# Optimization experiments

Measured on AMD Instinct MI355X. Metric: run time of the kernel, lower is better.

Reference implementation:

```python
import jax, jax.numpy as jnp
import numpy as np

B, C, H, W, K, NH = 4, 128, 64, 64, 7, 8
DH = C // NH          # per-head dim
PAD = (K - 1) // 2    # symmetric padding since K is odd


def setup_inputs() -> dict:
    key = jax.random.key(0)
    ks = jax.random.split(key, 9)
    s = 1.0 / np.sqrt(C)
    f32 = jnp.float32
    return {
        "x": jax.random.normal(ks[0], (B, C, H, W), f32),
        "wq": jax.random.normal(ks[1], (C, C), f32) * s,
        "bq": jax.random.normal(ks[2], (C,), f32) * 0.01,
        "wk": jax.random.normal(ks[3], (C, C), f32) * s,
        "bk": jax.random.normal(ks[4], (C,), f32) * 0.01,
        "wv": jax.random.normal(ks[5], (C, C), f32) * s,
        "bv": jax.random.normal(ks[6], (C,), f32) * 0.01,
        "pos_h": jax.random.normal(ks[7], (NH, K), f32) * 0.02,
        "pos_w": jax.random.normal(ks[8], (NH, K), f32) * 0.02,
    }


def _unfold(p):
    # p: [B,C,H+K-1,W+K-1] -> [B,C,H,W,K,K] (KxK neighborhood per pixel),
    # matching torch .unfold(2,K,1).unfold(3,K,1). Loop is over fixed kernel size only.
    p1 = jnp.stack([p[:, :, i:i + H, :] for i in range(K)], axis=-1)      # [B,C,H,W+K-1,K]
    return jnp.stack([p1[:, :, :, j:j + W, :] for j in range(K)], axis=-1)  # [B,C,H,W,K,K]


def reference(x, wq, bq, wk, bk, wv, bv, pos_h, pos_w):
    cx = x  # cx defaults to x in the original module
    pc = jnp.pad(cx, ((0, 0), (0, 0), (PAD, PAD), (PAD, PAD)))
    # 1x1 convs are pointwise channel mixes
    k = jnp.einsum('oc,bchw->bohw', wk, pc) + bk[None, :, None, None]
    v = jnp.einsum('oc,bchw->bohw', wv, pc) + bv[None, :, None, None]
    q = jnp.einsum('oc,bchw->bohw', wq, x) + bq[None, :, None, None]

    ku = _unfold(k).reshape(B, NH, DH, H, W, K, K)
    vu = _unfold(v).reshape(B, NH, DH, H, W, K, K)
    qh = q.reshape(B, NH, DH, H, W)

    # per-pixel logits over KxK neighborhood
    logits = jnp.einsum('bndhw,bndhwij->bnhwij', qh, ku)  # [B,NH,H,W,K,K]
    logits = logits + pos_h[None, :, None, None, :, None] + pos_w[None, :, None, None, None, :]

    weights = jax.nn.softmax(logits.reshape(B, NH, H, W, K * K), axis=-1)
    out = jnp.einsum('bnhwk,bndhwk->bndhw', weights, vu.reshape(B, NH, DH, H, W, K * K))
    return out.reshape(B, C, H, W)
```

## Files before the change

kernel.cpp:

```cpp
#include <hip/hip_runtime.h>
#include <cmath>

constexpr int Bn = 4, Cn = 128, Hn = 64, Wn = 64, Kn = 7, NHn = 8, DHn = 16, PADn = 3;
constexpr int HWn = Hn * Wn;
constexpr int TS = 16;
constexpr size_t QPLANE = (size_t)Bn * NHn * HWn * DHn;

constexpr int HR = 22;
constexpr int HC = 24;
constexpr int KP = 24;
constexpr int VW = 14;

typedef float f32x4 __attribute__((ext_vector_type(4)));
typedef short short8 __attribute__((ext_vector_type(8)));
typedef unsigned int u32x4 __attribute__((ext_vector_type(4)));
typedef unsigned short u16x4 __attribute__((ext_vector_type(4)));
typedef unsigned short u16x8 __attribute__((ext_vector_type(8)));

__device__ __forceinline__ unsigned short f32_to_bf16_rne(float f) {
  unsigned u = __float_as_uint(f);
  unsigned r = u + 0x7fffu + ((u >> 16) & 1u);
  return (unsigned short)(r >> 16);
}
__device__ __forceinline__ float bf16_to_f32(unsigned short h) {
  return __uint_as_float(((unsigned)h) << 16);
}
__device__ __forceinline__ unsigned pk_bf16(float lo, float hi) {
  return (__float_as_uint(lo) >> 16) | (__float_as_uint(hi) & 0xffff0000u);
}
__device__ __forceinline__ f32x4 max4(f32x4 a, f32x4 b) {
  a[0] = fmaxf(a[0], b[0]); a[1] = fmaxf(a[1], b[1]);
  a[2] = fmaxf(a[2], b[2]); a[3] = fmaxf(a[3], b[3]);
  return a;
}

union UVcast { u32x4 u; short8 s; };

__global__ __launch_bounds__(256)
void prep(const float* __restrict__ x,
          const float* __restrict__ wq, const float* __restrict__ wk,
          const float* __restrict__ wv,
          unsigned short* __restrict__ Whl, unsigned short* __restrict__ xThl)
{
  const int t = threadIdx.x;
  if (blockIdx.z == 4) {
    if (blockIdx.y != 0 || blockIdx.x >= 48) return;
    const int mat = blockIdx.x >> 4;
    const int chunk = blockIdx.x & 15;
    const float* W = (mat == 0) ? wq : (mat == 1) ? wk : wv;
    const int i = (chunk * 256 + t) * 4;
    const f32x4 v = *reinterpret_cast<const f32x4*>(W + i);
    unsigned short h[4], l[4];
#pragma unroll
    for (int j = 0; j < 4; ++j) {
      h[j] = f32_to_bf16_rne(v[j]);
      l[j] = f32_to_bf16_rne(v[j] - bf16_to_f32(h[j]));
    }
    unsigned short* base = Whl + (size_t)mat * 2 * 16384;
    *reinterpret_cast<uint2*>(base + i) =
        make_uint2(h[0] | ((unsigned)h[1] << 16), h[2] | ((unsigned)h[3] << 16));
    *reinterpret_cast<uint2*>(base + 16384 + i) =
        make_uint2(l[0] | ((unsigned)l[1] << 16), l[2] | ((unsigned)l[3] << 16));
    return;
  }

  __shared__ float sm[32][65];
  const int b   = blockIdx.z;
  const int c0g = blockIdx.y * 32;
  const int p0g = blockIdx.x * 64;
  const float* xb = x + (size_t)b * Cn * HWn;

#pragma unroll
  for (int rep = 0; rep < 2; ++rep) {
    const int cl = rep * 16 + (t >> 4);
    const int pl = (t & 15) * 4;
    const f32x4 v = *reinterpret_cast<const f32x4*>(xb + (size_t)(c0g + cl) * HWn + p0g + pl);
    sm[cl][pl + 0] = v[0]; sm[cl][pl + 1] = v[1];
    sm[cl][pl + 2] = v[2]; sm[cl][pl + 3] = v[3];
  }
  __syncthreads();

  const int pl = t >> 2;
  const int c0 = (t & 3) * 8;
  u32x4 hw, lw;
#pragma unroll
  for (int j = 0; j < 4; ++j) {
    const float v0 = sm[c0 + 2 * j][pl];
    const float v1 = sm[c0 + 2 * j + 1][pl];
    const unsigned short h0 = f32_to_bf16_rne(v0);
    const unsigned short h1 = f32_to_bf16_rne(v1);
    const unsigned short l0 = f32_to_bf16_rne(v0 - bf16_to_f32(h0));
    const unsigned short l1 = f32_to_bf16_rne(v1 - bf16_to_f32(h1));
    hw[j] = h0 | ((unsigned)h1 << 16);
    lw[j] = l0 | ((unsigned)l1 << 16);
  }
  unsigned short* dst = xThl + (size_t)b * 2 * HWn * Cn + (size_t)(p0g + pl) * Cn + c0g + c0;
  *reinterpret_cast<u32x4*>(dst)            = hw;
  *reinterpret_cast<u32x4*>(dst + HWn * Cn) = lw;
}

__global__ __launch_bounds__(64)
void qkv_mfma(const unsigned short* __restrict__ Whl,
              const unsigned short* __restrict__ xThl,
              const float* __restrict__ bq_, const float* __restrict__ bk_,
              const float* __restrict__ bv_,
              unsigned short* __restrict__ qo, unsigned short* __restrict__ kbf,
              unsigned short* __restrict__ vbf)
{
  const int z   = blockIdx.z;
  const int mat = z >> 2;
  const int b   = z & 3;
  const float* bias = (mat == 0) ? bq_ : (mat == 1) ? bk_ : bv_;

  const int lane = threadIdx.x;
  const int r    = lane & 15;
  const int quad = lane >> 4;
  const int mbase = blockIdx.y * 64;
  const int nbase = blockIdx.x * 64;

  const unsigned short* Wm = Whl  + (size_t)mat * 2 * Cn * Cn;
  const unsigned short* Xb = xThl + (size_t)b   * 2 * HWn * Cn;

  f32x4 acc[4][4] = {};

#pragma unroll
  for (int ks = 0; ks < 4; ++ks) {
    const int kk = ks * 32 + quad * 8;
    short8 Ah[4], Al[4], Bh[4], Bl[4];
#pragma unroll
    for (int mt = 0; mt < 4; ++mt) {
      const unsigned short* p = Wm + (size_t)(mbase + mt * 16 + r) * Cn + kk;
      Ah[mt] = *reinterpret_cast<const short8*>(p);
      Al[mt] = *reinterpret_cast<const short8*>(p + Cn * Cn);
    }
#pragma unroll
    for (int nt = 0; nt < 4; ++nt) {
      const unsigned short* p = Xb + (size_t)(nbase + nt * 16 + r) * Cn + kk;
      Bh[nt] = *reinterpret_cast<const short8*>(p);
      Bl[nt] = *reinterpret_cast<const short8*>(p + HWn * Cn);
    }
#pragma unroll
    for (int mt = 0; mt < 4; ++mt)
#pragma unroll
      for (int nt = 0; nt < 4; ++nt) {
        acc[mt][nt] = __builtin_amdgcn_mfma_f32_16x16x32_bf16(Ah[mt], Bh[nt], acc[mt][nt], 0, 0, 0);
        acc[mt][nt] = __builtin_amdgcn_mfma_f32_16x16x32_bf16(Ah[mt], Bl[nt], acc[mt][nt], 0, 0, 0);
        acc[mt][nt] = __builtin_amdgcn_mfma_f32_16x16x32_bf16(Al[mt], Bh[nt], acc[mt][nt], 0, 0, 0);
      }
  }

#pragma unroll
  for (int mt = 0; mt < 4; ++mt) {
    const int n = blockIdx.y * 4 + mt;
    const f32x4 b4 = *reinterpret_cast<const f32x4*>(bias + mbase + mt * 16 + quad * 4);
#pragma unroll
    for (int nt = 0; nt < 4; ++nt) {
      const int p = nbase + nt * 16 + r;
      const size_t off = ((size_t)((b * NHn + n) * HWn + p)) * DHn + quad * 4;
      f32x4 val = acc[mt][nt] + b4;
      if (mat == 0) {
        u16x4 hi4, lo4;
#pragma unroll
        for (int j = 0; j < 4; ++j) {
          const unsigned short hb = f32_to_bf16_rne(val[j]);
          hi4[j] = hb;
          lo4[j] = f32_to_bf16_rne(val[j] - bf16_to_f32(hb));
        }
        *reinterpret_cast<u16x4*>(qo + off)          = hi4;
        *reinterpret_cast<u16x4*>(qo + QPLANE + off) = lo4;
      } else {
        unsigned short* y = (mat == 1) ? kbf : vbf;
        u16x4 pkv;
        pkv[0] = f32_to_bf16_rne(val[0]); pkv[1] = f32_to_bf16_rne(val[1]);
        pkv[2] = f32_to_bf16_rne(val[2]); pkv[3] = f32_to_bf16_rne(val[3]);
        *reinterpret_cast<u16x4*>(y + off) = pkv;
      }
    }
  }
}

__global__ __launch_bounds__(256)
void sasa_attn(const unsigned short* __restrict__ qhl,
               const unsigned short* __restrict__ kbf,
               const unsigned short* __restrict__ vbf,
               const float* __restrict__ bk_, const float* __restrict__ bv_,
               const float* __restrict__ pos_h, const float* __restrict__ pos_w,
               float* __restrict__ out)
{
  __shared__ __align__(16) unsigned short ksm[HR * HC * KP];
  __shared__ __align__(16) unsigned       vsm[HR * DHn * VW];

  const int z  = blockIdx.z;
  const int b  = z >> 3;
  const int n  = z & 7;
  const int h0 = blockIdx.y * TS;
  const int w0 = blockIdx.x * TS;
  const int tid  = threadIdx.x;
  const int lane = tid & 63;
  const int wv   = tid >> 6;
  const int r    = lane & 15;
  const int quad = lane >> 4;
  const int cbase = n * DHn;

  const unsigned short* kb = kbf + ((size_t)(b * NHn + n) * HWn) * DHn;
  const unsigned short* vb = vbf + ((size_t)(b * NHn + n) * HWn) * DHn;
  const size_t qbase = ((size_t)(b * NHn + n) * HWn) * DHn;
  const unsigned short* qhp = qhl + qbase;
  const unsigned short* qlp = qhl + QPLANE + qbase;

  u16x8 kb0, kb1, vb0, vb1;
#pragma unroll
  for (int j = 0; j < 8; ++j) {
    kb0[j] = f32_to_bf16_rne(bk_[cbase + j]);
    kb1[j] = f32_to_bf16_rne(bk_[cbase + 8 + j]);
    vb0[j] = f32_to_bf16_rne(bv_[cbase + j]);
    vb1[j] = f32_to_bf16_rne(bv_[cbase + 8 + j]);
  }

  for (int c = tid; c < HR * HC * 2; c += 256) {
    const int pix  = c >> 1;
    const int half = c & 1;
    const int hh = pix / HC;
    const int ww = pix - hh * HC;
    const int gh = h0 + hh - PADn;
    const int gw = w0 + ww - PADn;
    const bool inb = (gh >= 0) && (gh < Hn) && (gw >= 0) && (gw < Wn);
    u16x8 kd;
    if (inb) kd = *reinterpret_cast<const u16x8*>(kb + ((size_t)(gh * Wn + gw)) * DHn + half * 8);
    else     kd = half ? kb1 : kb0;
    *reinterpret_cast<u16x8*>(ksm + pix * KP + half * 8) = kd;
  }

  for (int pp = tid; pp < HR * (HC / 2); pp += 256) {
    const int hh = pp / (HC / 2);
    const int wp = pp - hh * (HC / 2);
    const int gh = h0 + hh - PADn;
    u16x8 a0, a1, c0, c1;
    {
      const int gw = w0 + 2 * wp - PADn;
      const bool inb = (gh >= 0) && (gh < Hn) && (gw >= 0) && (gw < Wn);
      if (inb) {
        const size_t src = ((size_t)(gh * Wn + gw)) * DHn;
        a0 = *reinterpret_cast<const u16x8*>(vb + src);
        a1 = *reinterpret_cast<const u16x8*>(vb + src + 8);
      } else { a0 = vb0; a1 = vb1; }
    }
    {
      const int gw = w0 + 2 * wp + 1 - PADn;
      const bool inb = (gh >= 0) && (gh < Hn) && (gw >= 0) && (gw < Wn);
      if (inb) {
        const size_t src = ((size_t)(gh * Wn + gw)) * DHn;
        c0 = *reinterpret_cast<const u16x8*>(vb + src);
        c1 = *reinterpret_cast<const u16x8*>(vb + src + 8);
      } else { c0 = vb0; c1 = vb1; }
    }
    unsigned* dst = vsm + (hh * DHn) * VW + wp;
#pragma unroll
    for (int d = 0; d < 8; ++d)
      dst[d * VW] = (unsigned)(unsigned short)a0[d] | ((unsigned)(unsigned short)c0[d] << 16);
#pragma unroll
    for (int d = 0; d < 8; ++d)
      dst[(8 + d) * VW] = (unsigned)(unsigned short)a1[d] | ((unsigned)(unsigned short)c1[d] << 16);
  }

  float ph[7];
#pragma unroll
  for (int i = 0; i < 7; ++i) ph[i] = pos_h[n * Kn + i];
  f32x4 pw4[2];
#pragma unroll
  for (int win = 0; win < 2; ++win) {
#pragma unroll
    for (int reg = 0; reg < 4; ++reg) {
      const int ww = win * 8 + 4 * quad + reg;
      const int j  = ww - r;
      const bool valid = (j >= 0) && (j < 7) && (win == 0 || ww >= 16);
      const int jc = j < 0 ? 0 : (j > 6 ? 6 : j);
      const float pv = pos_w[n * Kn + jc];
      pw4[win][reg] = valid ? pv : -1e30f;
    }
  }

  __syncthreads();

  const f32x4 zero4 = {};
  for (int hl = 0; hl < 4; ++hl) {
    const int h = wv * 4 + hl;

    const int pix = (h0 + h) * Wn + (w0 + r);
    const unsigned short* qsel = (quad < 2) ? qhp : qlp;
    const short8 qf = *reinterpret_cast<const short8*>(qsel + (size_t)pix * DHn + (quad & 1) * 8);

    f32x4 L[14];
#pragma unroll
    for (int i = 0; i < 7; ++i) {
#pragma unroll
      for (int win = 0; win < 2; ++win) {
        const short8 kf = *reinterpret_cast<const short8*>(
            ksm + ((h + i) * HC + win * 8 + r) * KP + (quad & 1) * 8);
        f32x4 d = __builtin_amdgcn_mfma_f32_16x16x32_bf16(kf, qf, zero4, 0, 0, 0);
        d = d + pw4[win];
        d = d + (f32x4)ph[i];
        L[i * 2 + win] = d;
      }
    }

    f32x4 M4 = L[0];
#pragma unroll
    for (int t = 1; t < 14; ++t) M4 = max4(M4, L[t]);
    float m = fmaxf(fmaxf(M4[0], M4[1]), fmaxf(M4[2], M4[3]));
    m = fmaxf(m, __shfl_xor(m, 16, 64));
    m = fmaxf(m, __shfl_xor(m, 32, 64));

    f32x4 S4 = {};
#pragma unroll
    for (int t = 0; t < 14; ++t) {
      f32x4 e;
      e[0] = __expf(L[t][0] - m);
      e[1] = __expf(L[t][1] - m);
      e[2] = __expf(L[t][2] - m);
      e[3] = __expf(L[t][3] - m);
      L[t] = e;
      S4 += e;
    }
    float s = (S4[0] + S4[1]) + (S4[2] + S4[3]);
    s += __shfl_xor(s, 16, 64);
    s += __shfl_xor(s, 32, 64);
    const float inv = 1.0f / s;

    f32x4 oA = {}, oB = {};
#pragma unroll
    for (int i = 0; i < 7; ++i) {
      const f32x4 e0 = L[2 * i]     * (f32x4)inv;
      const f32x4 e1 = L[2 * i + 1] * (f32x4)inv;
      UVcast A;
      A.u[0] = pk_bf16(e0[0], e0[1]);
      A.u[1] = pk_bf16(e0[2], e0[3]);
      A.u[2] = pk_bf16(e1[0], e1[1]);
      A.u[3] = pk_bf16(e1[2], e1[3]);

      const unsigned* vp = vsm + ((h + i) * DHn + r) * VW + 2 * quad;
      const uint2 v0 = *reinterpret_cast<const uint2*>(vp);
      const uint2 v1 = *reinterpret_cast<const uint2*>(vp + 4);
      UVcast Bv;
      Bv.u[0] = v0.x; Bv.u[1] = v0.y; Bv.u[2] = v1.x; Bv.u[3] = v1.y;

      f32x4& acc = (i & 1) ? oB : oA;
      acc = __builtin_amdgcn_mfma_f32_16x16x32_bf16(A.s, Bv.s, acc, 0, 0, 0);
    }
    const f32x4 O = oA + oB;

    float* op = out + ((size_t)(b * Cn + cbase + r)) * HWn + (h0 + h) * Wn + w0 + 4 * quad;
    *reinterpret_cast<f32x4*>(op) = O;
  }
}

extern "C" void kernel_launch(void* const* d_in, const int* in_sizes, int n_in,
                              void* d_out, int out_size, void* d_ws, size_t ws_size,
                              hipStream_t stream) {
  const float* x     = (const float*)d_in[0];
  const float* wq    = (const float*)d_in[1];
  const float* bq    = (const float*)d_in[2];
  const float* wk    = (const float*)d_in[3];
  const float* bk    = (const float*)d_in[4];
  const float* wv    = (const float*)d_in[5];
  const float* bv    = (const float*)d_in[6];
  const float* pos_h = (const float*)d_in[7];
  const float* pos_w = (const float*)d_in[8];
  float* out = (float*)d_out;

  const size_t tensor_elems = (size_t)Bn * Cn * HWn;
  unsigned short* qhl  = (unsigned short*)d_ws;
  unsigned short* kbf  = qhl + 2 * tensor_elems;
  unsigned short* vbf  = kbf + tensor_elems;
  unsigned short* Whl  = vbf + tensor_elems;
  unsigned short* xThl = Whl + (size_t)3 * 2 * Cn * Cn;

  dim3 gp(HWn / 64, Cn / 32, Bn + 1);
  prep<<<gp, 256, 0, stream>>>(x, wq, wk, wv, Whl, xThl);

  dim3 g1(HWn / 64, Cn / 64, 3 * Bn);
  qkv_mfma<<<g1, 64, 0, stream>>>(Whl, xThl, bq, bk, bv, qhl, kbf, vbf);

  dim3 g2(Wn / TS, Hn / TS, Bn * NHn);
  sasa_attn<<<g2, 256, 0, stream>>>(qhl, kbf, vbf, bk, bv, pos_h, pos_w, out);
}
```

Before: 111.5 us.

## Fuse x/weight bf16 split prep into QKV MFMA kernel using LDS-staged x tile

Result: faster. 107.0 us, median of 2 (-4.0%).

```diff
diff --git a/kernel.cpp b/kernel.cpp
--- a/kernel.cpp
+++ b/kernel.cpp
@@ -5,6 +5,9 @@
 constexpr int HWn = Hn * Wn;
 constexpr int TS = 16;
 constexpr size_t QPLANE = (size_t)Bn * NHn * HWn * DHn;
+
+constexpr int SP   = 64;
+constexpr int XROW = 136;
 
 constexpr int HR = 22;
 constexpr int HC = 24;
@@ -36,90 +39,75 @@
 
 union UVcast { u32x4 u; short8 s; };
 
-__global__ __launch_bounds__(256)
-void prep(const float* __restrict__ x,
-          const float* __restrict__ wq, const float* __restrict__ wk,
-          const float* __restrict__ wv,
-          unsigned short* __restrict__ Whl, unsigned short* __restrict__ xThl)
+__global__ __launch_bounds__(512)
+void qkv_fused(const float* __restrict__ x,
+               const float* __restrict__ wq, const float* __restrict__ wk,
+               const float* __restrict__ wv,
+               const float* __restrict__ bq_, const float* __restrict__ bk_,
+               const float* __restrict__ bv_,
+               unsigned short* __restrict__ qo, unsigned short* __restrict__ kbf,
+               unsigned short* __restrict__ vbf)
 {
-  const int t = threadIdx.x;
-  if (blockIdx.z == 4) {
-    if (blockIdx.y != 0 || blockIdx.x >= 48) return;
-    const int mat = blockIdx.x >> 4;
-    const int chunk = blockIdx.x & 15;
-    const float* W = (mat == 0) ? wq : (mat == 1) ? wk : wv;
-    const int i = (chunk * 256 + t) * 4;
-    const f32x4 v = *reinterpret_cast<const f32x4*>(W + i);
-    unsigned short h[4], l[4];
-#pragma unroll
-    for (int j = 0; j < 4; ++j) {
-      h[j] = f32_to_bf16_rne(v[j]);
-      l[j] = f32_to_bf16_rne(v[j] - bf16_to_f32(h[j]));
-    }
-    unsigned short* base = Whl + (size_t)mat * 2 * 16384;
-    *reinterpret_cast<uint2*>(base + i) =
-        make_uint2(h[0] | ((unsigned)h[1] << 16), h[2] | ((unsigned)h[3] << 16));
-    *reinterpret_cast<uint2*>(base + 16384 + i) =
-        make_uint2(l[0] | ((unsigned)l[1] << 16), l[2] | ((unsigned)l[3] << 16));
-    return;
-  }
-
-  __shared__ float sm[32][65];
+  __shared__ float smf[32][SP + 1];
+  __shared__ __align__(16) unsigned short xthi[SP * XROW];
+  __shared__ __align__(16) unsigned short xtlo[SP * XROW];
+
   const int b   = blockIdx.z;
-  const int c0g = blockIdx.y * 32;
-  const int p0g = blockIdx.x * 64;
+  const int p0  = blockIdx.x * SP;
+  const int tid = threadIdx.x;
   const float* xb = x + (size_t)b * Cn * HWn;
 
-#pragma unroll
-  for (int rep = 0; rep < 2; ++rep) {
-    const int cl = rep * 16 + (t >> 4);
-    const int pl = (t & 15) * 4;
-    const f32x4 v = *reinterpret_cast<const f32x4*>(xb + (size_t)(c0g + cl) * HWn + p0g + pl);
-    sm[cl][pl + 0] = v[0]; sm[cl][pl + 1] = v[1];
-    sm[cl][pl + 2] = v[2]; sm[cl][pl + 3] = v[3];
-  }
-  __syncthreads();
-
-  const int pl = t >> 2;
-  const int c0 = (t & 3) * 8;
-  u32x4 hw, lw;
-#pragma unroll
-  for (int j = 0; j < 4; ++j) {
-    const float v0 = sm[c0 + 2 * j][pl];
-    const float v1 = sm[c0 + 2 * j + 1][pl];
-    const unsigned short h0 = f32_to_bf16_rne(v0);
-    const unsigned short h1 = f32_to_bf16_rne(v1);
-    const unsigned short l0 = f32_to_bf16_rne(v0 - bf16_to_f32(h0));
-    const unsigned short l1 = f32_to_bf16_rne(v1 - bf16_to_f32(h1));
-    hw[j] = h0 | ((unsigned)h1 << 16);
-    lw[j] = l0 | ((unsigned)l1 << 16);
-  }
-  unsigned short* dst = xThl + (size_t)b * 2 * HWn * Cn + (size_t)(p0g + pl) * Cn + c0g + c0;
-  *reinterpret_cast<u32x4*>(dst)            = hw;
-  *reinterpret_cast<u32x4*>(dst + HWn * Cn) = lw;
-}
-
-__global__ __launch_bounds__(64)
-void qkv_mfma(const unsigned short* __restrict__ Whl,
-              const unsigned short* __restrict__ xThl,
-              const float* __restrict__ bq_, const float* __restrict__ bk_,
-              const float* __restrict__ bv_,
-              unsigned short* __restrict__ qo, unsigned short* __restrict__ kbf,
-              unsigned short* __restrict__ vbf)
-{
-  const int z   = blockIdx.z;
-  const int mat = z >> 2;
-  const int b   = z & 3;
-  const float* bias = (mat == 0) ? bq_ : (mat == 1) ? bk_ : bv_;
-
-  const int lane = threadIdx.x;
+  f32x4 xr0, xr1, xr2, xr3;
+  {
+    const int c  = tid >> 4;
+    const int p4 = (tid & 15) * 4;
+    const float* bp = xb + (size_t)c * HWn + p0 + p4;
+    xr0 = *reinterpret_cast<const f32x4*>(bp);
+    xr1 = *reinterpret_cast<const f32x4*>(bp + (size_t)32 * HWn);
+    xr2 = *reinterpret_cast<const f32x4*>(bp + (size_t)64 * HWn);
+    xr3 = *reinterpret_cast<const f32x4*>(bp + (size_t)96 * HWn);
+  }
+
+#pragma unroll
+  for (int cc = 0; cc < 4; ++cc) {
+    const f32x4 v = (cc == 0) ? xr0 : (cc == 1) ? xr1 : (cc == 2) ? xr2 : xr3;
+    const int cl = tid >> 4;
+    const int p4 = (tid & 15) * 4;
+    smf[cl][p4 + 0] = v[0]; smf[cl][p4 + 1] = v[1];
+    smf[cl][p4 + 2] = v[2]; smf[cl][p4 + 3] = v[3];
+    __syncthreads();
+    if (tid < 256) {
+      const int pl  = tid >> 2;
+      const int c0l = (tid & 3) * 8;
+      u32x4 hw, lw;
+#pragma unroll
+      for (int j = 0; j < 4; ++j) {
+        const float v0 = smf[c0l + 2 * j][pl];
+        const float v1 = smf[c0l + 2 * j + 1][pl];
+        const unsigned short h0 = f32_to_bf16_rne(v0);
+        const unsigned short h1 = f32_to_bf16_rne(v1);
+        const unsigned short l0 = f32_to_bf16_rne(v0 - bf16_to_f32(h0));
+        const unsigned short l1 = f32_to_bf16_rne(v1 - bf16_to_f32(h1));
+        hw[j] = h0 | ((unsigned)h1 << 16);
+        lw[j] = l0 | ((unsigned)l1 << 16);
+      }
+      const int csw = (cc * 32 + c0l) ^ ((pl & 7) << 3);
+      *reinterpret_cast<u32x4*>(xthi + pl * XROW + csw) = hw;
+      *reinterpret_cast<u32x4*>(xtlo + pl * XROW + csw) = lw;
+    }
+    __syncthreads();
+  }
+
+  const int wave = tid >> 6;
+  if (wave >= 6) return;
+  const int lane = tid & 63;
   const int r    = lane & 15;
   const int quad = lane >> 4;
-  const int mbase = blockIdx.y * 64;
-  const int nbase = blockIdx.x * 64;
-
-  const unsigned short* Wm = Whl  + (size_t)mat * 2 * Cn * Cn;
-  const unsigned short* Xb = xThl + (size_t)b   * 2 * HWn * Cn;
+  const int mat  = wave >> 1;
+  const int half = wave & 1;
+  const int mbase = half * 64;
+  const float* Wsel = (mat == 0) ? wq : (mat == 1) ? wk : wv;
+  const float* bias = (mat == 0) ? bq_ : (mat == 1) ? bk_ : bv_;
 
   f32x4 acc[4][4] = {};
 
@@ -129,15 +117,30 @@
     short8 Ah[4], Al[4], Bh[4], Bl[4];
 #pragma unroll
     for (int mt = 0; mt < 4; ++mt) {
-      const unsigned short* p = Wm + (size_t)(mbase + mt * 16 + r) * Cn + kk;
-      Ah[mt] = *reinterpret_cast<const short8*>(p);
-      Al[mt] = *reinterpret_cast<const short8*>(p + Cn * Cn);
+      const float* wp = Wsel + (size_t)(mbase + mt * 16 + r) * Cn + kk;
+      const f32x4 wa = *reinterpret_cast<const f32x4*>(wp);
+      const f32x4 wb = *reinterpret_cast<const f32x4*>(wp + 4);
+      short8 ah, al;
+#pragma unroll
+      for (int j = 0; j < 4; ++j) {
+        const unsigned short h = f32_to_bf16_rne(wa[j]);
+        ah[j] = (short)h;
+        al[j] = (short)f32_to_bf16_rne(wa[j] - bf16_to_f32(h));
+      }
+#pragma unroll
+      for (int j = 0; j < 4; ++j) {
+        const unsigned short h = f32_to_bf16_rne(wb[j]);
+        ah[4 + j] = (short)h;
+        al[4 + j] = (short)f32_to_bf16_rne(wb[j] - bf16_to_f32(h));
+      }
+      Ah[mt] = ah; Al[mt] = al;
     }
 #pragma unroll
     for (int nt = 0; nt < 4; ++nt) {
-      const unsigned short* p = Xb + (size_t)(nbase + nt * 16 + r) * Cn + kk;
-      Bh[nt] = *reinterpret_cast<const short8*>(p);
-      Bl[nt] = *reinterpret_cast<const short8*>(p + HWn * Cn);
+      const int px  = nt * 16 + r;
+      const int csw = kk ^ ((px & 7) << 3);
+      Bh[nt] = *reinterpret_cast<const short8*>(xthi + px * XROW + csw);
+      Bl[nt] = *reinterpret_cast<const short8*>(xtlo + px * XROW + csw);
     }
 #pragma unroll
     for (int mt = 0; mt < 4; ++mt)
@@ -151,11 +154,11 @@
 
 #pragma unroll
   for (int mt = 0; mt < 4; ++mt) {
-    const int n = blockIdx.y * 4 + mt;
+    const int n = half * 4 + mt;
     const f32x4 b4 = *reinterpret_cast<const f32x4*>(bias + mbase + mt * 16 + quad * 4);
 #pragma unroll
     for (int nt = 0; nt < 4; ++nt) {
-      const int p = nbase + nt * 16 + r;
+      const int p = p0 + nt * 16 + r;
       const size_t off = ((size_t)((b * NHn + n) * HWn + p)) * DHn + quad * 4;
       f32x4 val = acc[mt][nt] + b4;
       if (mat == 0) {
@@ -369,17 +372,12 @@
   float* out = (float*)d_out;
 
   const size_t tensor_elems = (size_t)Bn * Cn * HWn;
-  unsigned short* qhl  = (unsigned short*)d_ws;
-  unsigned short* kbf  = qhl + 2 * tensor_elems;
-  unsigned short* vbf  = kbf + tensor_elems;
-  unsigned short* Whl  = vbf + tensor_elems;
-  unsigned short* xThl = Whl + (size_t)3 * 2 * Cn * Cn;
-
-  dim3 gp(HWn / 64, Cn / 32, Bn + 1);
-  prep<<<gp, 256, 0, stream>>>(x, wq, wk, wv, Whl, xThl);
-
-  dim3 g1(HWn / 64, Cn / 64, 3 * Bn);
-  qkv_mfma<<<g1, 64, 0, stream>>>(Whl, xThl, bq, bk, bv, qhl, kbf, vbf);
+  unsigned short* qhl = (unsigned short*)d_ws;
+  unsigned short* kbf = qhl + 2 * tensor_elems;
+  unsigned short* vbf = kbf + tensor_elems;
+
+  dim3 gq(HWn / SP, 1, Bn);
+  qkv_fused<<<gq, 512, 0, stream>>>(x, wq, wk, wv, bq, bk, bv, qhl, kbf, vbf);
 
   dim3 g2(Wn / TS, Hn / TS, Bn * NHn);
   sasa_attn<<<g2, 256, 0, stream>>>(qhl, kbf, vbf, bk, bv, pos_h, pos_w, out);
```
